# Optimization experiments

Hardware: AMD Instinct MI355X
Metric: run time of the kernel (lower is better)

Reference implementation:

```python
import jax, jax.numpy as jnp
import numpy as np
from jax import lax

B, C, H, W, K = 16, 64, 192, 192, 11
EPS = 1e-5


def _depthwise(x, w, pad):
    # x: (B,C,h,w), w: (C,1,kh,kw), pad: ((ph,ph),(pw,pw))
    return lax.conv_general_dilated(
        x, w, window_strides=(1, 1), padding=pad,
        feature_group_count=x.shape[1],
        dimension_numbers=('NCHW', 'OIHW', 'NCHW'))


def _maxpool3(x):
    return lax.reduce_window(x, -jnp.inf, lax.max,
                             (1, 1, 3, 3), (1, 1, 1, 1),
                             ((0, 0), (0, 0), (1, 1), (1, 1)))


def _blurpool(x):
    # filt_size=4, stride=3, reflect pad (1,2) on each spatial dim
    a = jnp.array([1., 3., 3., 1.], dtype=x.dtype)
    f = a[:, None] * a[None, :]
    f = f / f.sum()
    filt = jnp.tile(f[None, None], (x.shape[1], 1, 1, 1))  # (C,1,4,4)
    xp = jnp.pad(x, ((0, 0), (0, 0), (1, 2), (1, 2)), mode='reflect')
    return lax.conv_general_dilated(
        xp, filt, window_strides=(3, 3), padding='VALID',
        feature_group_count=x.shape[1],
        dimension_numbers=('NCHW', 'OIHW', 'NCHW'))


def _h_transform(x):
    b, c, h, w = x.shape
    x = jnp.pad(x, ((0, 0), (0, 0), (0, 0), (0, w)))
    x = x.reshape(b, c, -1)[..., :-w]
    return x.reshape(b, c, h, 2 * w - 1)


def _inv_h_transform(x):
    b, c, h, l = x.shape
    x = x.reshape(b, c, -1)
    x = jnp.pad(x, ((0, 0), (0, 0), (0, h)))
    x = x.reshape(b, c, h, 2 * h)
    return x[..., :h]


def _v_transform(x):
    return _h_transform(x.transpose(0, 1, 3, 2)).transpose(0, 1, 3, 2)


def _inv_v_transform(x):
    return _inv_h_transform(x.transpose(0, 1, 3, 2)).transpose(0, 1, 3, 2)


def _mra(x, w_h1, w_v1, w_h2, w_v2, bn_gamma, bn_beta, bn_mean, bn_var):
    kp = K // 2
    x_tem = _blurpool(_maxpool3(x))                 # (B,C,h,h), h=64
    x_h1 = _depthwise(x_tem, w_h1, ((kp, kp), (1, 1)))
    x_w1 = _depthwise(x_tem, w_v1, ((1, 1), (kp, kp)))
    x_h2 = _inv_h_transform(_depthwise(_h_transform(x_tem), w_h2, ((kp, kp), (1, 1))))
    x_w2 = _inv_v_transform(_depthwise(_v_transform(x_tem), w_v2, ((1, 1), (kp, kp))))
    att = x_h1 + x_w1 + x_h2 + x_w2
    # inference-mode BatchNorm2d
    inv = bn_gamma / jnp.sqrt(bn_var + EPS)
    att = att * inv[None, :, None, None] + (bn_beta - bn_mean * inv)[None, :, None, None]
    gate = jax.nn.sigmoid(att)                      # (B,C,h,h)
    # nearest-neighbor upsample to (H,W): torch idx = floor(i*h/H)
    h = gate.shape[-2]
    ih = (jnp.arange(H) * h) // H
    iw = (jnp.arange(W) * gate.shape[-1]) // W
    gate_up = gate[:, :, ih][:, :, :, iw]           # (B,C,H,W)
    return x[:, :C] * gate_up


def setup_inputs() -> dict:
    key = jax.random.key(0)
    ks = jax.random.split(key, 9)
    x = jax.random.normal(ks[0], (B, C, H, W), jnp.float32)
    w_h1 = jax.random.normal(ks[1], (C, 1, K, 3), jnp.float32) * 0.05
    w_v1 = jax.random.normal(ks[2], (C, 1, 3, K), jnp.float32) * 0.05
    w_h2 = jax.random.normal(ks[3], (C, 1, K, 3), jnp.float32) * 0.05
    w_v2 = jax.random.normal(ks[4], (C, 1, 3, K), jnp.float32) * 0.05
    bn_gamma = jnp.ones((C,), jnp.float32)
    bn_beta = jnp.zeros((C,), jnp.float32)
    bn_mean = jax.random.normal(ks[5], (C,), jnp.float32) * 0.1
    bn_var = jax.random.uniform(ks[6], (C,), jnp.float32, 0.5, 1.5)
    return {'x': x, 'w_h1': w_h1, 'w_v1': w_v1, 'w_h2': w_h2, 'w_v2': w_v2,
            'bn_gamma': bn_gamma, 'bn_beta': bn_beta,
            'bn_mean': bn_mean, 'bn_var': bn_var}


def reference(x, w_h1, w_v1, w_h2, w_v2, bn_gamma, bn_beta, bn_mean, bn_var):
    return _mra(x, w_h1, w_v1, w_h2, w_v2, bn_gamma, bn_beta, bn_mean, bn_var)
```

## Files before the change

kernel.cpp:

```cpp
#include <hip/hip_runtime.h>
#include <math.h>

__global__ __launch_bounds__(256, 4) void mra_fused(
    const float* __restrict__ x,
    const float* __restrict__ wh1g, const float* __restrict__ wv1g,
    const float* __restrict__ wh2g, const float* __restrict__ wv2g,
    const float* __restrict__ gamma, const float* __restrict__ beta,
    const float* __restrict__ mean, const float* __restrict__ var,
    float* __restrict__ out) {
    const int plane = blockIdx.x;
    const int c = plane & 63;
    __shared__ float T[64 * 80];
    __shared__ float att[64 * 64];

    for (int e = threadIdx.x; e < 64 * 80; e += 256) T[e] = 0.f;
    __syncthreads();

    const int j = threadIdx.x & 63;
    const int il = threadIdx.x >> 6;

    {
        float* xs = att;
        const float* xp = x + (size_t)plane * 36864;

        int colk[6];
#pragma unroll
        for (int k = 0; k < 6; ++k)
            colk[k] = min(max(3 * j - 2 + k, 0), 191);

        for (int chunk = 0; chunk < 16; ++chunk) {
            const int i0 = chunk * 4;
            const int base = 3 * i0 - 2;
            for (int f = threadIdx.x; f < 15 * 48; f += 256) {
                int r = f / 48, c4 = f - r * 48;
                int src = min(max(base + r, 0), 191);
                ((float4*)xs)[f] = ((const float4*)(xp + (size_t)src * 192))[c4];
            }
            __syncthreads();

            const int i = i0 + il;
            float vmu[4][6];
#pragma unroll
            for (int k = 0; k < 6; ++k) {
                const float* cp = xs + 3 * il * 192 + colk[k];
                float p0 = cp[0 * 192], p1 = cp[1 * 192], p2 = cp[2 * 192];
                float p3 = cp[3 * 192], p4 = cp[4 * 192], p5 = cp[5 * 192];
                float q1 = fmaxf(p1, p2), q2 = fmaxf(p2, p3);
                float q3 = fmaxf(p3, p4), q4 = fmaxf(p4, p5);
                vmu[0][k] = fmaxf(p0, q1);
                vmu[1][k] = fmaxf(p1, q2);
                vmu[2][k] = fmaxf(p2, q3);
                vmu[3][k] = fmaxf(p3, q4);
            }
            float cbv[4];
#pragma unroll
            for (int u = 0; u < 4; ++u) {
                float g1 = fmaxf(vmu[u][1], vmu[u][2]);
                float g2 = fmaxf(vmu[u][2], vmu[u][3]);
                float g3 = fmaxf(vmu[u][3], vmu[u][4]);
                float g4 = fmaxf(vmu[u][4], vmu[u][5]);
                float h0 = fmaxf(vmu[u][0], g1);
                float h1 = fmaxf(vmu[u][1], g2);
                float h2 = fmaxf(vmu[u][2], g3);
                float h3 = fmaxf(vmu[u][3], g4);
                float ha = (j == 0) ? h2 : h0;
                cbv[u] = ha + 3.f * h1 + 3.f * h2 + h3;
            }
            float c0 = (i == 0) ? cbv[2] : cbv[0];
            float acc = c0 + 3.f * cbv[1] + 3.f * cbv[2] + cbv[3];
            T[i * 80 + 6 + j] = acc * (1.f / 64.f);
            __syncthreads();
        }
    }

    const float inv = gamma[c] * rsqrtf(var[c] + 1e-5f);
    const float bias = beta[c] - mean[c] * inv;

    const int ib = il * 16;
    const int t0 = ib - 6;

    float Wa[33], Wb[33];
    float racc[13];

#pragma unroll
    for (int k = 0; k < 33; ++k) {
        Wa[k] = wh1g[c * 33 + k];
        Wb[k] = wh2g[c * 33 + k];
    }
#pragma unroll
    for (int k = 0; k < 13; ++k) racc[k] = 0.f;
#pragma unroll
    for (int tt = 0; tt < 28; ++tt) {
        const int t = t0 + tt;
        if (t >= 0 && t < 64) {
            float w_[13];
#pragma unroll
            for (int d = 0; d < 13; ++d) w_[d] = T[t * 80 + j + d];
#pragma unroll
            for (int p = 0; p < 11; ++p) {
                racc[(tt + 11 - p) % 13] +=
                    Wa[p * 3 + 0] * w_[5] + Wa[p * 3 + 1] * w_[6] +
                    Wa[p * 3 + 2] * w_[7] +
                    Wb[p * 3 + 0] * w_[10 - p] +
                    Wb[p * 3 + 1] * w_[11 - p] +
                    Wb[p * 3 + 2] * w_[12 - p];
            }
        }
        if (tt >= 12) {
            const int i = t - 6;
            att[i * 64 + j] = racc[tt % 13];
        }
        racc[tt % 13] = 0.f;
    }

#pragma unroll
    for (int k = 0; k < 33; ++k) {
        Wa[k] = wv1g[c * 33 + k];
        Wb[k] = wv2g[c * 33 + k];
    }
#pragma unroll
    for (int k = 0; k < 13; ++k) racc[k] = 0.f;
#pragma unroll
    for (int tt = 0; tt < 28; ++tt) {
        const int t = t0 + tt;
        if (t >= 0 && t < 64) {
            float w_[13];
#pragma unroll
            for (int d = 0; d < 13; ++d) w_[d] = T[t * 80 + j + d];
#pragma unroll
            for (int p = 0; p < 3; ++p) {
#pragma unroll
                for (int q = 0; q < 11; ++q) {
                    racc[(tt + 7 - p) % 13] += Wa[p * 11 + q] * w_[q + 1];
                    racc[(tt + 2 - p + q) % 13] += Wb[p * 11 + q] * w_[q + 1];
                }
            }
        }
        if (tt >= 12) {
            const int i = t - 6;
            float z = (att[i * 64 + j] + racc[tt % 13]) * inv + bias;
            att[i * 64 + j] = 1.f / (1.f + __expf(-z));
        }
        racc[tt % 13] = 0.f;
    }
    __syncthreads();

    const float4* xp4 = (const float4*)(x + (size_t)plane * 36864);
    float4* op4 = (float4*)(out + (size_t)plane * 36864);
#pragma unroll
    for (int bse = 0; bse < 9216; bse += 1024) {
        float4 xv[4];
        int e[4];
#pragma unroll
        for (int u = 0; u < 4; ++u) {
            e[u] = bse + u * 256 + threadIdx.x;
            xv[u] = xp4[e[u]];
        }
#pragma unroll
        for (int u = 0; u < 4; ++u) {
            int i = e[u] / 48, c4 = e[u] - i * 48;
            const float* gp = att + (i / 3) * 64;
            int jj = 4 * c4;
            int g0 = jj / 3;
            int r = jj - 3 * g0;
            float ga = gp[g0], gb = gp[g0 + 1];
            float4 o;
            o.x = xv[u].x * ga;
            o.y = xv[u].y * (r == 2 ? gb : ga);
            o.z = xv[u].z * (r == 0 ? ga : gb);
            o.w = xv[u].w * gb;
            op4[e[u]] = o;
        }
    }
}

extern "C" void kernel_launch(void* const* d_in, const int* in_sizes, int n_in,
                              void* d_out, int out_size, void* d_ws, size_t ws_size,
                              hipStream_t stream) {
    const float* x     = (const float*)d_in[0];
    const float* wh1   = (const float*)d_in[1];
    const float* wv1   = (const float*)d_in[2];
    const float* wh2   = (const float*)d_in[3];
    const float* wv2   = (const float*)d_in[4];
    const float* gamma = (const float*)d_in[5];
    const float* beta  = (const float*)d_in[6];
    const float* mean  = (const float*)d_in[7];
    const float* var   = (const float*)d_in[8];
    float* out  = (float*)d_out;

    mra_fused<<<1024, 256, 0, stream>>>(x, wh1, wv1, wh2, wv2,
                                        gamma, beta, mean, var, out);
}
```

Measured before the change: 311.9 us.

## Fuse gated upsample output into vertical conv loop and drop pooling LDS staging

The maxpool+blurpool stage now has each wavefront read its input rows straight from global memory into a rolling register window. This replaces the block-wide shared-memory staging and its per-chunk barriers. The final gate-multiply-and-store pass is folded into the second convolution loop, so each gate row is applied to its three upsampled output rows as soon as it is computed. That removes a separate pass and a block barrier, and lets the global loads and stores overlap with the conv arithmetic. The cost is strided, less coalesced global reads during pooling, and a correctness dependence on wave64 lockstep for gate rows shared within a wavefront.

```diff
diff --git a/kernel.cpp b/kernel.cpp
--- a/kernel.cpp
+++ b/kernel.cpp
@@ -11,72 +11,95 @@
     const int plane = blockIdx.x;
     const int c = plane & 63;
     __shared__ float T[64 * 80];
-    __shared__ float att[64 * 64];
-
-    for (int e = threadIdx.x; e < 64 * 80; e += 256) T[e] = 0.f;
-    __syncthreads();
+    __shared__ float gateL[64 * 64];
 
     const int j = threadIdx.x & 63;
     const int il = threadIdx.x >> 6;
+    const int ib = il * 16;
 
     {
-        float* xs = att;
-        const float* xp = x + (size_t)plane * 36864;
-
+        float4 z4 = make_float4(0.f, 0.f, 0.f, 0.f);
+        float4* t4 = (float4*)(T + ib * 80);
+#pragma unroll
+        for (int u = 0; u < 5; ++u) t4[u * 64 + j] = z4;
+    }
+
+    const float* xp = x + (size_t)plane * 36864;
+
+    {
         int colk[6];
 #pragma unroll
         for (int k = 0; k < 6; ++k)
             colk[k] = min(max(3 * j - 2 + k, 0), 191);
 
-        for (int chunk = 0; chunk < 16; ++chunk) {
-            const int i0 = chunk * 4;
-            const int base = 3 * i0 - 2;
-            for (int f = threadIdx.x; f < 15 * 48; f += 256) {
-                int r = f / 48, c4 = f - r * 48;
-                int src = min(max(base + r, 0), 191);
-                ((float4*)xs)[f] = ((const float4*)(xp + (size_t)src * 192))[c4];
-            }
-            __syncthreads();
-
-            const int i = i0 + il;
-            float vmu[4][6];
-#pragma unroll
-            for (int k = 0; k < 6; ++k) {
-                const float* cp = xs + 3 * il * 192 + colk[k];
-                float p0 = cp[0 * 192], p1 = cp[1 * 192], p2 = cp[2 * 192];
-                float p3 = cp[3 * 192], p4 = cp[4 * 192], p5 = cp[5 * 192];
-                float q1 = fmaxf(p1, p2), q2 = fmaxf(p2, p3);
-                float q3 = fmaxf(p3, p4), q4 = fmaxf(p4, p5);
-                vmu[0][k] = fmaxf(p0, q1);
-                vmu[1][k] = fmaxf(p1, q2);
-                vmu[2][k] = fmaxf(p2, q3);
-                vmu[3][k] = fmaxf(p3, q4);
-            }
-            float cbv[4];
-#pragma unroll
-            for (int u = 0; u < 4; ++u) {
-                float g1 = fmaxf(vmu[u][1], vmu[u][2]);
-                float g2 = fmaxf(vmu[u][2], vmu[u][3]);
-                float g3 = fmaxf(vmu[u][3], vmu[u][4]);
-                float g4 = fmaxf(vmu[u][4], vmu[u][5]);
-                float h0 = fmaxf(vmu[u][0], g1);
-                float h1 = fmaxf(vmu[u][1], g2);
-                float h2 = fmaxf(vmu[u][2], g3);
-                float h3 = fmaxf(vmu[u][3], g4);
-                float ha = (j == 0) ? h2 : h0;
-                cbv[u] = ha + 3.f * h1 + 3.f * h2 + h3;
-            }
-            float c0 = (i == 0) ? cbv[2] : cbv[0];
-            float acc = c0 + 3.f * cbv[1] + 3.f * cbv[2] + cbv[3];
-            T[i * 80 + 6 + j] = acc * (1.f / 64.f);
-            __syncthreads();
-        }
-    }
+        float rw[6][6];
+#pragma unroll
+        for (int s = 0; s < 6; ++s) {
+            const float* rp = xp + (size_t)min(max(3 * ib - 2 + s, 0), 191) * 192;
+#pragma unroll
+            for (int k = 0; k < 6; ++k) rw[s][k] = rp[colk[k]];
+        }
+
+#define POOL_EMIT(I, S0, S1, S2, S3, S4, S5)                              \
+        {                                                                 \
+            float cbv[4];                                                 \
+            {                                                             \
+                float vmu[4][6];                                          \
+                _Pragma("unroll") for (int k = 0; k < 6; ++k) {           \
+                    float p0 = rw[S0][k], p1 = rw[S1][k], p2 = rw[S2][k]; \
+                    float p3 = rw[S3][k], p4 = rw[S4][k], p5 = rw[S5][k]; \
+                    float q1 = fmaxf(p1, p2), q2 = fmaxf(p2, p3);         \
+                    float q3 = fmaxf(p3, p4), q4 = fmaxf(p4, p5);         \
+                    vmu[0][k] = fmaxf(p0, q1);                            \
+                    vmu[1][k] = fmaxf(p1, q2);                            \
+                    vmu[2][k] = fmaxf(p2, q3);                            \
+                    vmu[3][k] = fmaxf(p3, q4);                            \
+                }                                                         \
+                _Pragma("unroll") for (int u = 0; u < 4; ++u) {           \
+                    float g1 = fmaxf(vmu[u][1], vmu[u][2]);               \
+                    float g2 = fmaxf(vmu[u][2], vmu[u][3]);               \
+                    float g3 = fmaxf(vmu[u][3], vmu[u][4]);               \
+                    float g4 = fmaxf(vmu[u][4], vmu[u][5]);               \
+                    float h0 = fmaxf(vmu[u][0], g1);                      \
+                    float h1 = fmaxf(vmu[u][1], g2);                      \
+                    float h2 = fmaxf(vmu[u][2], g3);                      \
+                    float h3 = fmaxf(vmu[u][3], g4);                      \
+                    float ha = (j == 0) ? h2 : h0;       \
+                    cbv[u] = ha + 3.f * h1 + 3.f * h2 + h3;               \
+                }                                                         \
+            }                                                             \
+            float c0 = ((I) == 0) ? cbv[2] : cbv[0];     \
+            float accv = c0 + 3.f * cbv[1] + 3.f * cbv[2] + cbv[3];       \
+            T[(I) * 80 + 6 + j] = accv * (1.f / 64.f);                    \
+        }
+
+#define LOAD3(BR, S0, S1, S2)                                             \
+        {                                                                 \
+            const float* rp0 = xp + (size_t)min((BR), 191) * 192;         \
+            const float* rp1 = xp + (size_t)min((BR) + 1, 191) * 192;     \
+            const float* rp2 = xp + (size_t)min((BR) + 2, 191) * 192;     \
+            _Pragma("unroll") for (int k = 0; k < 6; ++k) {               \
+                rw[S0][k] = rp0[colk[k]];                                 \
+                rw[S1][k] = rp1[colk[k]];                                 \
+                rw[S2][k] = rp2[colk[k]];                                 \
+            }                                                             \
+        }
+
+#pragma unroll 1
+        for (int ii = 0; ii < 16; ii += 2) {
+            const int i = ib + ii;
+            POOL_EMIT(i, 0, 1, 2, 3, 4, 5);
+            LOAD3(3 * i + 4, 0, 1, 2);
+            POOL_EMIT(i + 1, 3, 4, 5, 0, 1, 2);
+            if (ii < 14) LOAD3(3 * i + 7, 3, 4, 5);
+        }
+#undef POOL_EMIT
+#undef LOAD3
+    }
+    __syncthreads();
 
     const float inv = gamma[c] * rsqrtf(var[c] + 1e-5f);
     const float bias = beta[c] - mean[c] * inv;
-
-    const int ib = il * 16;
     const int t0 = ib - 6;
 
     float Wa[33], Wb[33];
@@ -106,11 +129,18 @@
                     Wb[p * 3 + 2] * w_[12 - p];
             }
         }
-        if (tt >= 12) {
-            const int i = t - 6;
-            att[i * 64 + j] = racc[tt % 13];
-        }
+        if (tt >= 12) gateL[(ib + tt - 12) * 64 + j] = racc[tt % 13];
         racc[tt % 13] = 0.f;
+    }
+
+    int g0s[3], rs[3];
+#pragma unroll
+    for (int u = 0; u < 3; ++u) {
+        int m = j + 64 * u;
+        int c4 = m % 48;
+        int jj = 4 * c4;
+        g0s[u] = jj / 3;
+        rs[u] = jj - 3 * (jj / 3);
     }
 
 #pragma unroll
@@ -120,6 +150,8 @@
     }
 #pragma unroll
     for (int k = 0; k < 13; ++k) racc[k] = 0.f;
+    const float4* xp4 = (const float4*)xp;
+    float4* op4 = (float4*)(out + (size_t)plane * 36864);
 #pragma unroll
     for (int tt = 0; tt < 28; ++tt) {
         const int t = t0 + tt;
@@ -137,40 +169,45 @@
             }
         }
         if (tt >= 12) {
-            const int i = t - 6;
-            float z = (att[i * 64 + j] + racc[tt % 13]) * inv + bias;
-            att[i * 64 + j] = 1.f / (1.f + __expf(-z));
+            const int i = ib + tt - 12;
+            const int fb = i * 144;
+            float4 xv0 = xp4[fb + j];
+            float4 xv1 = xp4[fb + 64 + j];
+            float4 xv2;
+            if (j < 16) xv2 = xp4[fb + 128 + j];
+            float z = (gateL[i * 64 + j] + racc[tt % 13]) * inv + bias;
+            float g = 1.f / (1.f + __expf(-z));
+            gateL[i * 64 + j] = g;
+            const float* gr = gateL + i * 64;
+            {
+                float ga = gr[g0s[0]], gb = gr[g0s[0] + 1];
+                float4 o;
+                o.x = xv0.x * ga;
+                o.y = xv0.y * (rs[0] == 2 ? gb : ga);
+                o.z = xv0.z * (rs[0] == 0 ? ga : gb);
+                o.w = xv0.w * gb;
+                op4[fb + j] = o;
+            }
+            {
+                float ga = gr[g0s[1]], gb = gr[g0s[1] + 1];
+                float4 o;
+                o.x = xv1.x * ga;
+                o.y = xv1.y * (rs[1] == 2 ? gb : ga);
+                o.z = xv1.z * (rs[1] == 0 ? ga : gb);
+                o.w = xv1.w * gb;
+                op4[fb + 64 + j] = o;
+            }
+            if (j < 16) {
+                float ga = gr[g0s[2]], gb = gr[g0s[2] + 1];
+                float4 o;
+                o.x = xv2.x * ga;
+                o.y = xv2.y * (rs[2] == 2 ? gb : ga);
+                o.z = xv2.z * (rs[2] == 0 ? ga : gb);
+                o.w = xv2.w * gb;
+                op4[fb + 128 + j] = o;
+            }
         }
         racc[tt % 13] = 0.f;
-    }
-    __syncthreads();
-
-    const float4* xp4 = (const float4*)(x + (size_t)plane * 36864);
-    float4* op4 = (float4*)(out + (size_t)plane * 36864);
-#pragma unroll
-    for (int bse = 0; bse < 9216; bse += 1024) {
-        float4 xv[4];
-        int e[4];
-#pragma unroll
-        for (int u = 0; u < 4; ++u) {
-            e[u] = bse + u * 256 + threadIdx.x;
-            xv[u] = xp4[e[u]];
-        }
-#pragma unroll
-        for (int u = 0; u < 4; ++u) {
-            int i = e[u] / 48, c4 = e[u] - i * 48;
-            const float* gp = att + (i / 3) * 64;
-            int jj = 4 * c4;
-            int g0 = jj / 3;
-            int r = jj - 3 * g0;
-            float ga = gp[g0], gb = gp[g0 + 1];
-            float4 o;
-            o.x = xv[u].x * ga;
-            o.y = xv[u].y * (r == 2 ? gb : ga);
-            o.z = xv[u].z * (r == 0 ? ga : gb);
-            o.w = xv[u].w * gb;
-            op4[e[u]] = o;
-        }
     }
 }
 
```

Measured after the change: 304.6 us. -2.3%, faster.
